# Optimization experiments

Measured on AMD Instinct MI355X. Metric: run time of the kernel, lower is better.

The kernel has to match this reference:

```python
import jax, jax.numpy as jnp
import numpy as np

S, B, E, H, NQ, V, T = 128, 128, 64, 8, 8, 30000, 12
N_RAND_OPS = 30


def _build_random_layer(n_wires, n_ops=N_RAND_OPS, seed=1234):
    # Deterministic stand-in for tq.RandomLayer(n_ops=30): random fixed-angle
    # rotations and CNOTs over the wires.
    rng = np.random.RandomState(seed)
    ops = []
    for _ in range(n_ops):
        kind = rng.randint(4)
        if kind == 3 and n_wires >= 2:
            c = int(rng.randint(n_wires))
            t = int(rng.randint(n_wires - 1))
            if t >= c:
                t += 1
            ops.append(('cnot', c, t, 0.0))
        else:
            g = ('rx', 'ry', 'rz')[kind % 3]
            ops.append((g, int(rng.randint(n_wires)), -1, float(rng.uniform(0.0, 2 * np.pi))))
    return ops

_RAND_OPS = _build_random_layer(H)


def _apply_rot(state, kind, theta, w):
    # state: (N, 2, 2, ..., 2); wire w lives on axis w+1. theta: scalar or (N,).
    th = jnp.asarray(theta, jnp.float32)
    if th.ndim == 1:
        th = th.reshape((-1,) + (1,) * (state.ndim - 2))
    th = th / 2
    a0 = jnp.take(state, 0, axis=w + 1)
    a1 = jnp.take(state, 1, axis=w + 1)
    c, s = jnp.cos(th), jnp.sin(th)
    if kind == 'rx':
        n0, n1 = c * a0 - 1j * s * a1, -1j * s * a0 + c * a1
    elif kind == 'ry':
        n0, n1 = c * a0 - s * a1, s * a0 + c * a1
    else:  # rz
        p = jnp.exp(-1j * th)
        n0, n1 = p * a0, jnp.conj(p) * a1
    return jnp.stack([n0, n1], axis=w + 1)


def _apply_cnot(state, c, t):
    s0 = jnp.take(state, 0, axis=c + 1)
    s1 = jnp.take(state, 1, axis=c + 1)
    t_ax = t + 1 if t < c else t  # target axis after removing control axis
    s1 = jnp.flip(s1, axis=t_ax)
    return jnp.stack([s0, s1], axis=c + 1)


def _measure_z(state):
    probs = jnp.real(state * jnp.conj(state))
    n = state.ndim - 1
    zs = []
    for w in range(n):
        d = jnp.take(probs, 0, axis=w + 1) - jnp.take(probs, 1, axis=w + 1)
        zs.append(d.sum(axis=tuple(range(1, d.ndim))))
    return jnp.stack(zs, axis=1)  # (N, n_wires)


def setup_inputs() -> dict:
    key = jax.random.key(0)
    ks = jax.random.split(key, 10)
    fan_lin = E + H
    return {
        'emb': jax.random.normal(ks[0], (V, E), jnp.float32),
        'Win': jax.random.normal(ks[1], (4, NQ, fan_lin), jnp.float32) / np.sqrt(fan_lin),
        'b_in': jax.random.normal(ks[2], (4, NQ), jnp.float32) * 0.1,
        'phi': jax.random.uniform(ks[3], (4, NQ), jnp.float32, 0.0, 2 * np.pi),
        'Wout': jax.random.normal(ks[4], (4, H, NQ), jnp.float32) / np.sqrt(NQ),
        'b_out': jax.random.normal(ks[5], (4, H), jnp.float32) * 0.1,
        'phiq': jax.random.uniform(ks[6], (H,), jnp.float32, 0.0, 2 * np.pi),
        'Whead': jax.random.normal(ks[7], (T, H), jnp.float32) / np.sqrt(H),
        'b_head': jax.random.normal(ks[8], (T,), jnp.float32) * 0.1,
        'sentence': jax.random.randint(ks[9], (S, B), 0, V, jnp.int64),
    }


def reference(emb, Win, b_in, phi, Wout, b_out, phiq, Whead, b_head, sentence):
    embeds = emb[sentence]  # (S, B, E)
    bsz = sentence.shape[1]
    h0 = jnp.zeros((bsz, H), emb.dtype)
    c0 = jnp.zeros_like(h0)

    def step(carry, x):
        hx, cx = carry
        comb = jnp.concatenate([x, hx], axis=1)  # (B, E+H)
        # QGate closed form: RX(z_i) encode + trainable RX(phi_i) + CNOT chain
        # gives <Z_k> = prod_{j<=k} cos(z_j + phi_j).
        z = jnp.einsum('bf,gqf->bgq', comb, Win) + b_in + phi  # (B,4,NQ)
        q = jnp.cumprod(jnp.cos(z), axis=-1)
        pre = jnp.einsum('bgq,ghq->bgh', q, Wout) + b_out      # (B,4,H)
        f = jax.nn.sigmoid(pre[:, 0])
        i = jax.nn.sigmoid(pre[:, 1])
        g = jnp.tanh(pre[:, 2])
        o = jax.nn.sigmoid(pre[:, 3])
        cx = f * cx + i * g
        hx = o * jnp.tanh(cx)
        return (hx, cx), hx

    _, outs = jax.lax.scan(step, (h0, c0), embeds)  # (S, B, H)
    flat = outs.transpose(1, 0, 2).reshape(-1, H)   # (B*S, H) batch-major (as in source)

    # QFC head: statevector simulation over H wires
    n = H
    N = flat.shape[0]
    state = jnp.zeros((N, 2 ** n), jnp.complex64).at[:, 0].set(1.0)
    state = state.reshape((N,) + (2,) * n)
    for w in range(n):
        state = _apply_rot(state, 'ry', flat[:, w], w)
    for name, a, b, ang in _RAND_OPS:
        if name == 'cnot':
            state = _apply_cnot(state, a, b)
        else:
            state = _apply_rot(state, name, ang, a)
    for w in range(n):
        state = _apply_rot(state, 'rx', phiq[w], w)
    zexp = _measure_z(state)                        # (B*S, H)
    logits = zexp @ Whead.T + b_head
    # faithful to source: view batch-major flat tensor as (seq, batch, T)
    logits = logits.reshape(S, B, T)
    return jax.nn.log_softmax(logits, axis=2)
```

## Files before the change

kernel.cpp:

```cpp
#include <hip/hip_runtime.h>
#include <math.h>
#include <stdint.h>

#define S_    128
#define B_    128
#define E_    64
#define H_    8
#define T_    12
#define FAN_  72
#define NOPS_ 30
#define MAXG_ 30
#define NROWS_ (S_ * B_)

constexpr double CT_PI = 3.14159265358979323846;

constexpr double ct_cos(double x) {
    double t = 1.0, s = 1.0, x2 = x * x;
    for (int k = 1; k <= 20; k++) { t *= -x2 / ((2.0*k - 1.0) * (2.0*k)); s += t; }
    return s;
}
constexpr double ct_sin(double x) {
    double t = x, s = x, x2 = x * x;
    for (int k = 1; k <= 20; k++) { t *= -x2 / ((2.0*k) * (2.0*k + 1.0)); s += t; }
    return s;
}

constexpr void ct_mmul(const double* A, const double* B, double* C) {
    for (int i = 0; i < 2; i++)
        for (int j = 0; j < 2; j++) {
            double rr = 0.0, ii = 0.0;
            for (int k = 0; k < 2; k++) {
                double ar = A[(i*2+k)*2], ai = A[(i*2+k)*2+1];
                double br = B[(k*2+j)*2], bi = B[(k*2+j)*2+1];
                rr += ar*br - ai*bi;
                ii += ar*bi + ai*br;
            }
            C[(i*2+j)*2] = rr; C[(i*2+j)*2+1] = ii;
        }
}

struct CTC {
    int n;
    int type[MAXG_];
    int w1[MAXG_];
    int w2[MAXG_];
    double U[MAXG_][8];
    double initM[8][8];
    double endM[8][8];
};

constexpr CTC build_ct() {
    uint32_t mt[624] = {};
    int idx = 624;
    {
        uint32_t s = 1234u;
        for (int i = 0; i < 624; i++) {
            mt[i] = s;
            s = 1812433253u * (s ^ (s >> 30)) + (uint32_t)i + 1u;
        }
    }
    auto nextf = [&]() -> uint32_t {
        if (idx >= 624) {
            for (int i = 0; i < 624; i++) {
                uint32_t y = (mt[i] & 0x80000000u) | (mt[(i+1)%624] & 0x7fffffffu);
                uint32_t v = mt[(i+397)%624] ^ (y >> 1);
                mt[i] = (y & 1u) ? (v ^ 0x9908b0dfu) : v;
            }
            idx = 0;
        }
        uint32_t y = mt[idx++];
        y ^= y >> 11;
        y ^= (y << 7)  & 0x9d2c5680u;
        y ^= (y << 15) & 0xefc60000u;
        y ^= y >> 18;
        return y;
    };
    auto randint = [&](uint32_t n) -> uint32_t {
        uint32_t rng = n - 1u, mask = rng;
        mask |= mask >> 1; mask |= mask >> 2; mask |= mask >> 4;
        mask |= mask >> 8; mask |= mask >> 16;
        uint32_t v = 0;
        do { v = nextf() & mask; } while (v > rng);
        return v;
    };
    auto uniform2pi = [&]() -> double {
        uint32_t a = nextf() >> 5;
        uint32_t b = nextf() >> 6;
        double d = ((double)a * 67108864.0 + (double)b) / 9007199254740992.0;
        return 2.0 * CT_PI * d;
    };

    int kindA[NOPS_] = {}, aA[NOPS_] = {}, bA[NOPS_] = {};
    double UA[NOPS_][8] = {};
    for (int i = 0; i < NOPS_; i++) {
        uint32_t kind = randint(4);
        if (kind == 3u) {
            int c = (int)randint(8);
            int t = (int)randint(7);
            if (t >= c) t += 1;
            kindA[i] = 1; aA[i] = c; bA[i] = t;
            UA[i][0] = 1.0; UA[i][6] = 1.0;
        } else {
            int g = (int)(kind % 3u);
            int w = (int)randint(8);
            double th = uniform2pi();
            double c = ct_cos(0.5 * th), s = ct_sin(0.5 * th);
            kindA[i] = 0; aA[i] = w; bA[i] = -1;
            if (g == 0)      { UA[i][0]=c;  UA[i][3]=-s; UA[i][5]=-s; UA[i][6]=c; }
            else if (g == 1) { UA[i][0]=c;  UA[i][2]=-s; UA[i][4]= s; UA[i][6]=c; }
            else             { UA[i][0]=c;  UA[i][1]=-s; UA[i][6]= c; UA[i][7]=s; }
        }
    }

    int ikind[MAXG_] = {}, ia[MAXG_] = {}, ib[MAXG_] = {};
    double iU[MAXG_][8] = {};
    int cnt = 0;
    double initM[8][8] = {}, endM[8][8] = {};
    for (int w = 0; w < 8; w++) { initM[w][0] = 1.0; initM[w][6] = 1.0;
                                  endM[w][0]  = 1.0; endM[w][6]  = 1.0; }

    for (int oi = 0; oi < NOPS_; oi++) {
        if (kindA[oi] == 0) {
            int w = aA[oi], k = cnt - 1;
            bool merged = false;
            while (k >= 0) {
                if (ikind[k] == 0) {
                    if (ia[k] == w) {
                        double tmp[8] = {};
                        ct_mmul(UA[oi], iU[k], tmp);
                        for (int j = 0; j < 8; j++) iU[k][j] = tmp[j];
                        merged = true; break;
                    }
                    k--;
                } else {
                    if (w == ia[k] || w == ib[k]) break;
                    k--;
                }
            }
            if (merged) continue;
            if (k < 0) {
                double tmp[8] = {};
                ct_mmul(UA[oi], initM[w], tmp);
                for (int j = 0; j < 8; j++) initM[w][j] = tmp[j];
                continue;
            }
            ikind[cnt] = 0; ia[cnt] = w; ib[cnt] = -1;
            for (int j = 0; j < 8; j++) iU[cnt][j] = UA[oi][j];
            cnt++;
        } else {
            int c = aA[oi], t2 = bA[oi], k = cnt - 1;
            bool cancelled = false;
            while (k >= 0) {
                if (ikind[k] == 0) {
                    int w = ia[k];
                    if (w == c || w == t2) break;
                    k--;
                } else {
                    int c2 = ia[k], tt = ib[k];
                    if (c2 == c && tt == t2) {
                        for (int m = k; m < cnt - 1; m++) {
                            ikind[m] = ikind[m+1]; ia[m] = ia[m+1]; ib[m] = ib[m+1];
                            for (int j = 0; j < 8; j++) iU[m][j] = iU[m+1][j];
                        }
                        cnt--; cancelled = true; break;
                    }
                    if (c2 != t2 && tt != c) k--;
                    else break;
                }
            }
            if (!cancelled) {
                ikind[cnt] = 1; ia[cnt] = c; ib[cnt] = t2;
                for (int j = 0; j < 8; j++) iU[cnt][j] = 0.0;
                iU[cnt][0] = 1.0; iU[cnt][6] = 1.0;
                cnt++;
            }
        }
    }
    bool blocked[8] = {};
    for (int k = cnt - 1; k >= 0; k--) {
        if (ikind[k] == 0) {
            int w = ia[k];
            if (!blocked[w]) {
                double tmp[8] = {};
                ct_mmul(endM[w], iU[k], tmp);
                for (int j = 0; j < 8; j++) endM[w][j] = tmp[j];
                for (int m = k; m < cnt - 1; m++) {
                    ikind[m] = ikind[m+1]; ia[m] = ia[m+1]; ib[m] = ib[m+1];
                    for (int j = 0; j < 8; j++) iU[m][j] = iU[m+1][j];
                }
                cnt--;
            }
        } else {
            blocked[ia[k]] = true; blocked[ib[k]] = true;
        }
    }

    CTC q = {};
    q.n = cnt;
    for (int i = 0; i < cnt; i++) {
        q.type[i] = ikind[i]; q.w1[i] = ia[i]; q.w2[i] = ib[i];
        for (int j = 0; j < 8; j++) q.U[i][j] = iU[i][j];
    }
    for (int w = 0; w < 8; w++)
        for (int j = 0; j < 8; j++) { q.initM[w][j] = initM[w][j]; q.endM[w][j] = endM[w][j]; }
    return q;
}

constexpr CTC CIRC = build_ct();

__device__ __forceinline__ float sigmoid_f(float x) { return 1.f / (1.f + __expf(-x)); }
__device__ __forceinline__ float tanh_f(float x) {
    float e = __expf(2.f * x);
    return 1.f - 2.f / (e + 1.f);
}

template<int CTRL>
__device__ __forceinline__ float dppf(float x) {
    union { float f; int i; } u, r;
    u.f = x;
    r.i = __builtin_amdgcn_update_dpp(0, u.i, CTRL, 0xF, 0xF, true);
    return r.f;
}

template<int M>
__device__ __forceinline__ float lane_xor(float x, int lane) {
    if constexpr (M == 1)  return dppf<0xB1>(x);
    else if constexpr (M == 2) return dppf<0x4E>(x);
    else if constexpr (M == 4) {
        float a = dppf<0x104>(x);
        float b = dppf<0x114>(x);
        return (lane & 4) ? b : a;
    }
    else if constexpr (M == 8) return dppf<0x128>(x);
    else return __shfl_xor(x, M, 64);
}

template<int W>
__device__ __forceinline__ float exch(float x, int lane) {
    if constexpr (W == 0) return __shfl_xor(x, 32, 64);
    else if constexpr (W == 1) return __shfl_xor(x, 16, 64);
    else if constexpr (W == 2) return lane_xor<8>(x, lane);
    else if constexpr (W == 3) return lane_xor<4>(x, lane);
    else if constexpr (W == 4) return lane_xor<2>(x, lane);
    else return lane_xor<1>(x, lane);
}

template<int W>
__device__ __forceinline__ int qbit_ct(int lane, int j) {
    if constexpr (W < 6) return (lane >> (5 - W)) & 1;
    else if constexpr (W == 6) return (j >> 1) & 1;
    else return j & 1;
}

__device__ __forceinline__ void pair_rt(float u0, float u1, float u2, float u3,
                                        float u4, float u5, float u6, float u7,
                                        float& a0r, float& a0i, float& a1r, float& a1i) {
    float n0r = u0*a0r - u1*a0i + u2*a1r - u3*a1i;
    float n0i = u0*a0i + u1*a0r + u2*a1i + u3*a1r;
    float n1r = u4*a0r - u5*a0i + u6*a1r - u7*a1i;
    float n1i = u4*a0i + u5*a0r + u6*a1i + u7*a1r;
    a0r = n0r; a0i = n0i; a1r = n1r; a1i = n1i;
}

template<int W>
__device__ __forceinline__ void gate_rt(float u0, float u1, float u2, float u3,
                                        float u4, float u5, float u6, float u7,
                                        int lane, float ar[4], float ai[4]) {
    if constexpr (W < 6) {
        const int b = (lane >> (5 - W)) & 1;
        const float dr  = b ? u6 : u0;
        const float di  = b ? u7 : u1;
        const float onr = b ? u4 : u2;
        const float oni = b ? u5 : u3;
        #pragma unroll
        for (int j = 0; j < 4; j++) {
            float br = exch<W>(ar[j], lane);
            float bi = exch<W>(ai[j], lane);
            float nr = dr * ar[j] - di * ai[j] + onr * br - oni * bi;
            float ni = dr * ai[j] + di * ar[j] + onr * bi + oni * br;
            ar[j] = nr; ai[j] = ni;
        }
    } else if constexpr (W == 6) {
        pair_rt(u0,u1,u2,u3,u4,u5,u6,u7, ar[0], ai[0], ar[2], ai[2]);
        pair_rt(u0,u1,u2,u3,u4,u5,u6,u7, ar[1], ai[1], ar[3], ai[3]);
    } else {
        pair_rt(u0,u1,u2,u3,u4,u5,u6,u7, ar[0], ai[0], ar[1], ai[1]);
        pair_rt(u0,u1,u2,u3,u4,u5,u6,u7, ar[2], ai[2], ar[3], ai[3]);
    }
}

template<int CW, int TW>
__device__ __forceinline__ void cnot_ct(int lane, float ar[4], float ai[4]) {
    if constexpr (TW < 6) {
        #pragma unroll
        for (int j = 0; j < 4; j++) {
            float br = exch<TW>(ar[j], lane);
            float bi = exch<TW>(ai[j], lane);
            int ctrl = qbit_ct<CW>(lane, j);
            ar[j] = ctrl ? br : ar[j];
            ai[j] = ctrl ? bi : ai[j];
        }
    } else if constexpr (TW == 6) {
        int cA = qbit_ct<CW>(lane, 0), cB = qbit_ct<CW>(lane, 1);
        float n0r = cA ? ar[2] : ar[0], n0i = cA ? ai[2] : ai[0];
        float n2r = cA ? ar[0] : ar[2], n2i = cA ? ai[0] : ai[2];
        float n1r = cB ? ar[3] : ar[1], n1i = cB ? ai[3] : ai[1];
        float n3r = cB ? ar[1] : ar[3], n3i = cB ? ai[1] : ai[3];
        ar[0]=n0r; ai[0]=n0i; ar[1]=n1r; ai[1]=n1i;
        ar[2]=n2r; ai[2]=n2i; ar[3]=n3r; ai[3]=n3i;
    } else {
        int cA = qbit_ct<CW>(lane, 0), cB = qbit_ct<CW>(lane, 2);
        float n0r = cA ? ar[1] : ar[0], n0i = cA ? ai[1] : ai[0];
        float n1r = cA ? ar[0] : ar[1], n1i = cA ? ai[0] : ai[1];
        float n2r = cB ? ar[3] : ar[2], n2i = cB ? ai[3] : ai[2];
        float n3r = cB ? ar[2] : ar[3], n3i = cB ? ai[2] : ai[3];
        ar[0]=n0r; ai[0]=n0i; ar[1]=n1r; ai[1]=n1i;
        ar[2]=n2r; ai[2]=n2i; ar[3]=n3r; ai[3]=n3i;
    }
}

template<int I>
__device__ __forceinline__ void gate_op(int lane, float ar[4], float ai[4]) {
    constexpr int w = CIRC.w1[I];
    constexpr float u0 = (float)CIRC.U[I][0], u1 = (float)CIRC.U[I][1];
    constexpr float u2 = (float)CIRC.U[I][2], u3 = (float)CIRC.U[I][3];
    constexpr float u4 = (float)CIRC.U[I][4], u5 = (float)CIRC.U[I][5];
    constexpr float u6 = (float)CIRC.U[I][6], u7 = (float)CIRC.U[I][7];
    gate_rt<w>(u0,u1,u2,u3,u4,u5,u6,u7, lane, ar, ai);
}

template<int I>
__device__ __forceinline__ void run_ops(int lane, float ar[4], float ai[4]) {
    if constexpr (I < CIRC.n) {
        if constexpr (CIRC.type[I] == 0) gate_op<I>(lane, ar, ai);
        else cnot_ct<CIRC.w1[I], CIRC.w2[I]>(lane, ar, ai);
        run_ops<I + 1>(lane, ar, ai);
    }
}

struct V2 { float r0, i0, r1, i1; };
template<int W>
__device__ __forceinline__ V2 init_wire(float th) {
    constexpr float m0 = (float)CIRC.initM[W][0], m1 = (float)CIRC.initM[W][1];
    constexpr float m2 = (float)CIRC.initM[W][2], m3 = (float)CIRC.initM[W][3];
    constexpr float m4 = (float)CIRC.initM[W][4], m5 = (float)CIRC.initM[W][5];
    constexpr float m6 = (float)CIRC.initM[W][6], m7 = (float)CIRC.initM[W][7];
    float c = __cosf(th), s = __sinf(th);
    V2 v;
    v.r0 = m0*c + m2*s; v.i0 = m1*c + m3*s;
    v.r1 = m4*c + m6*s; v.i1 = m5*c + m7*s;
    return v;
}

template<int W>
__device__ __forceinline__ void final_wire(float c, float s, int lane,
                                           float ar[4], float ai[4]) {
    constexpr float E0 = (float)CIRC.endM[W][0], E1 = (float)CIRC.endM[W][1];
    constexpr float E2 = (float)CIRC.endM[W][2], E3 = (float)CIRC.endM[W][3];
    constexpr float E4 = (float)CIRC.endM[W][4], E5 = (float)CIRC.endM[W][5];
    constexpr float E6 = (float)CIRC.endM[W][6], E7 = (float)CIRC.endM[W][7];
    float F0 =  c*E0 + s*E5;
    float F1 =  c*E1 - s*E4;
    float F2 =  c*E2 + s*E7;
    float F3 =  c*E3 - s*E6;
    float F4 =  s*E1 + c*E4;
    float F5 = -s*E0 + c*E5;
    float F6 =  s*E3 + c*E6;
    float F7 = -s*E2 + c*E7;
    gate_rt<W>(F0,F1,F2,F3,F4,F5,F6,F7, lane, ar, ai);
}

__device__ __forceinline__ void bcast8(float v, int lane, float h[8]) {
    float p  = lane_xor<1>(v, lane);
    float a0 = (lane & 1) ? p : v;
    float a1 = (lane & 1) ? v : p;
    float q0 = lane_xor<2>(a0, lane);
    float q1 = lane_xor<2>(a1, lane);
    float b0 = (lane & 2) ? q0 : a0;
    float b1 = (lane & 2) ? q1 : a1;
    float b2 = (lane & 2) ? a0 : q0;
    float b3 = (lane & 2) ? a1 : q1;
    float r0 = lane_xor<4>(b0, lane);
    float r1 = lane_xor<4>(b1, lane);
    float r2 = lane_xor<4>(b2, lane);
    float r3 = lane_xor<4>(b3, lane);
    h[0] = (lane & 4) ? r0 : b0;  h[1] = (lane & 4) ? r1 : b1;
    h[2] = (lane & 4) ? r2 : b2;  h[3] = (lane & 4) ? r3 : b3;
    h[4] = (lane & 4) ? b0 : r0;  h[5] = (lane & 4) ? b1 : r1;
    h[6] = (lane & 4) ? b2 : r2;  h[7] = (lane & 4) ? b3 : r3;
}

__device__ __forceinline__ void qfc_row(const float th[8],
    float cq[8], float sq[8], int lane,
    const float* __restrict__ Whead, const float* __restrict__ b_head,
    float* __restrict__ outrow)
{
    float ar[4], ai[4];
    {
        V2 v0 = init_wire<0>(th[0]);
        V2 v1 = init_wire<1>(th[1]);
        V2 v2 = init_wire<2>(th[2]);
        V2 v3 = init_wire<3>(th[3]);
        V2 v4 = init_wire<4>(th[4]);
        V2 v5 = init_wire<5>(th[5]);
        V2 v6 = init_wire<6>(th[6]);
        V2 v7 = init_wire<7>(th[7]);
        float Pr = 1.f, Pi = 0.f;
        {
            int bit = (lane >> 5) & 1;
            float er = bit ? v0.r1 : v0.r0, ei = bit ? v0.i1 : v0.i0;
            float nr = Pr*er - Pi*ei, ni = Pr*ei + Pi*er; Pr = nr; Pi = ni;
        }
        {
            int bit = (lane >> 4) & 1;
            float er = bit ? v1.r1 : v1.r0, ei = bit ? v1.i1 : v1.i0;
            float nr = Pr*er - Pi*ei, ni = Pr*ei + Pi*er; Pr = nr; Pi = ni;
        }
        {
            int bit = (lane >> 3) & 1;
            float er = bit ? v2.r1 : v2.r0, ei = bit ? v2.i1 : v2.i0;
            float nr = Pr*er - Pi*ei, ni = Pr*ei + Pi*er; Pr = nr; Pi = ni;
        }
        {
            int bit = (lane >> 2) & 1;
            float er = bit ? v3.r1 : v3.r0, ei = bit ? v3.i1 : v3.i0;
            float nr = Pr*er - Pi*ei, ni = Pr*ei + Pi*er; Pr = nr; Pi = ni;
        }
        {
            int bit = (lane >> 1) & 1;
            float er = bit ? v4.r1 : v4.r0, ei = bit ? v4.i1 : v4.i0;
            float nr = Pr*er - Pi*ei, ni = Pr*ei + Pi*er; Pr = nr; Pi = ni;
        }
        {
            int bit = lane & 1;
            float er = bit ? v5.r1 : v5.r0, ei = bit ? v5.i1 : v5.i0;
            float nr = Pr*er - Pi*ei, ni = Pr*ei + Pi*er; Pr = nr; Pi = ni;
        }
        float t0r = Pr*v6.r0 - Pi*v6.i0, t0i = Pr*v6.i0 + Pi*v6.r0;
        float t1r = Pr*v6.r1 - Pi*v6.i1, t1i = Pr*v6.i1 + Pi*v6.r1;
        ar[0] = t0r*v7.r0 - t0i*v7.i0;  ai[0] = t0r*v7.i0 + t0i*v7.r0;
        ar[1] = t0r*v7.r1 - t0i*v7.i1;  ai[1] = t0r*v7.i1 + t0i*v7.r1;
        ar[2] = t1r*v7.r0 - t1i*v7.i0;  ai[2] = t1r*v7.i0 + t1i*v7.r0;
        ar[3] = t1r*v7.r1 - t1i*v7.i1;  ai[3] = t1r*v7.i1 + t1i*v7.r1;
    }

    run_ops<0>(lane, ar, ai);

    final_wire<0>(cq[0], sq[0], lane, ar, ai);
    final_wire<1>(cq[1], sq[1], lane, ar, ai);
    final_wire<2>(cq[2], sq[2], lane, ar, ai);
    final_wire<3>(cq[3], sq[3], lane, ar, ai);
    final_wire<4>(cq[4], sq[4], lane, ar, ai);
    final_wire<5>(cq[5], sq[5], lane, ar, ai);
    final_wire<6>(cq[6], sq[6], lane, ar, ai);
    final_wire<7>(cq[7], sq[7], lane, ar, ai);

    float p0 = ar[0]*ar[0] + ai[0]*ai[0];
    float p1 = ar[1]*ar[1] + ai[1]*ai[1];
    float p2 = ar[2]*ar[2] + ai[2]*ai[2];
    float p3 = ar[3]*ar[3] + ai[3]*ai[3];
    float pt = p0 + p1 + p2 + p3;
    float a6 = p0 + p1 - p2 - p3;
    float a7 = p0 - p1 + p2 - p3;
    {
        float tv;
        tv = lane_xor<1>(pt, lane);  pt = (lane & 1)  ? (tv - pt) : (tv + pt);
        tv = lane_xor<2>(pt, lane);  pt = (lane & 2)  ? (tv - pt) : (tv + pt);
        tv = lane_xor<4>(pt, lane);  pt = (lane & 4)  ? (tv - pt) : (tv + pt);
        tv = lane_xor<8>(pt, lane);  pt = (lane & 8)  ? (tv - pt) : (tv + pt);
        tv = lane_xor<16>(pt, lane); pt = (lane & 16) ? (tv - pt) : (tv + pt);
        tv = lane_xor<32>(pt, lane); pt = (lane & 32) ? (tv - pt) : (tv + pt);
        a6 += lane_xor<1>(a6, lane);  a6 += lane_xor<2>(a6, lane);
        a6 += lane_xor<4>(a6, lane);  a6 += lane_xor<8>(a6, lane);
        a6 += lane_xor<16>(a6, lane); a6 += lane_xor<32>(a6, lane);
        a7 += lane_xor<1>(a7, lane);  a7 += lane_xor<2>(a7, lane);
        a7 += lane_xor<4>(a7, lane);  a7 += lane_xor<8>(a7, lane);
        a7 += lane_xor<16>(a7, lane); a7 += lane_xor<32>(a7, lane);
    }
    float zl[8];
    zl[0] = __shfl(pt, 32, 64);
    zl[1] = __shfl(pt, 16, 64);
    zl[2] = __shfl(pt, 8, 64);
    zl[3] = __shfl(pt, 4, 64);
    zl[4] = __shfl(pt, 2, 64);
    zl[5] = __shfl(pt, 1, 64);
    zl[6] = a6;
    zl[7] = a7;

    float logit = -1e30f;
    if (lane < T_) {
        logit = b_head[lane];
        #pragma unroll
        for (int w = 0; w < 8; w++)
            logit = fmaf(zl[w], Whead[lane * 8 + w], logit);
    }
    float mx = logit;
    mx = fmaxf(mx, lane_xor<1>(mx, lane));
    mx = fmaxf(mx, lane_xor<2>(mx, lane));
    mx = fmaxf(mx, lane_xor<4>(mx, lane));
    mx = fmaxf(mx, lane_xor<8>(mx, lane));
    float e = (lane < T_) ? __expf(logit - mx) : 0.f;
    float se = e;
    se += lane_xor<1>(se, lane);
    se += lane_xor<2>(se, lane);
    se += lane_xor<4>(se, lane);
    se += lane_xor<8>(se, lane);
    if (lane < T_)
        outrow[lane] = logit - mx - __logf(se);
}

__global__ __launch_bounds__(256) void k_lstm(
    const float* __restrict__ emb,
    const int* __restrict__ sentence,
    const float* __restrict__ Win,
    const float* __restrict__ b_in,
    const float* __restrict__ phi,
    const float* __restrict__ Wout,
    const float* __restrict__ b_out,
    float* __restrict__ angles)
{
    __shared__ float zxs[S_][32];

    const int t  = threadIdx.x;
    const int hw = t >> 5;
    const int l  = t & 31;
    const int b  = blockIdx.x;

    {
        const float4* w4 = (const float4*)(Win + l * FAN_);
        const float cb = b_in[l] + phi[l];

        #pragma unroll
        for (int kk = 0; kk < 4; kk++) {
            const int sb = hw * 16 + kk * 4;
            const float4* e4_0 = (const float4*)(emb + sentence[(sb + 0) * B_ + b] * E_);
            const float4* e4_1 = (const float4*)(emb + sentence[(sb + 1) * B_ + b] * E_);
            const float4* e4_2 = (const float4*)(emb + sentence[(sb + 2) * B_ + b] * E_);
            const float4* e4_3 = (const float4*)(emb + sentence[(sb + 3) * B_ + b] * E_);
            float a0 = cb, a1 = cb, a2 = cb, a3 = cb;
            #pragma unroll
            for (int f = 0; f < 16; f++) {
                float4 wv = w4[f];
                float4 x0 = e4_0[f];
                float4 x1 = e4_1[f];
                float4 x2 = e4_2[f];
                float4 x3 = e4_3[f];
                a0 = fmaf(x0.x, wv.x, a0); a0 = fmaf(x0.y, wv.y, a0);
                a0 = fmaf(x0.z, wv.z, a0); a0 = fmaf(x0.w, wv.w, a0);
                a1 = fmaf(x1.x, wv.x, a1); a1 = fmaf(x1.y, wv.y, a1);
                a1 = fmaf(x1.z, wv.z, a1); a1 = fmaf(x1.w, wv.w, a1);
                a2 = fmaf(x2.x, wv.x, a2); a2 = fmaf(x2.y, wv.y, a2);
                a2 = fmaf(x2.z, wv.z, a2); a2 = fmaf(x2.w, wv.w, a2);
                a3 = fmaf(x3.x, wv.x, a3); a3 = fmaf(x3.y, wv.y, a3);
                a3 = fmaf(x3.z, wv.z, a3); a3 = fmaf(x3.w, wv.w, a3);
            }
            zxs[sb + 0][l] = a0;
            zxs[sb + 1][l] = a1;
            zxs[sb + 2][l] = a2;
            zxs[sb + 3][l] = a3;
        }
    }
    __syncthreads();

    if (t < 32) {
        const int g = t >> 3;
        const int h = t & 7;
        const int q = t & 7;
        float wh[8], wo[8];
        #pragma unroll
        for (int k = 0; k < 8; k++) wh[k] = Win[t * FAN_ + 64 + k];
        #pragma unroll
        for (int k = 0; k < 8; k++) wo[k] = Wout[(g * 8 + h) * 8 + k];
        const float bo = b_out[g * 8 + h];

        float hxv[8];
        #pragma unroll
        for (int k = 0; k < 8; k++) hxv[k] = 0.f;
        float cx = 0.f;

        for (int s = 0; s < S_; s++) {
            float z = zxs[s][t];
            #pragma unroll
            for (int k = 0; k < 8; k++) z = fmaf(wh[k], hxv[k], z);

            float qc = __cosf(z);
            float u1 = dppf<0x111>(qc); qc = (q >= 1) ? qc * u1 : qc;
            float u2 = dppf<0x112>(qc); qc = (q >= 2) ? qc * u2 : qc;
            float u4 = dppf<0x114>(qc); qc = (q >= 4) ? qc * u4 : qc;

            float qch[8];
            bcast8(qc, t, qch);
            float pre = bo;
            #pragma unroll
            for (int qq = 0; qq < 8; qq++) pre = fmaf(wo[qq], qch[qq], pre);

            float e1 = lane_xor<8>(pre, t);
            float e2 = __shfl_xor(pre, 16, 64);
            float e3 = __shfl_xor(e1, 16, 64);
            float p0 = (g==0)?pre:(g==1)?e1:(g==2)?e2:e3;
            float p1 = (g==1)?pre:(g==0)?e1:(g==3)?e2:e3;
            float p2 = (g==2)?pre:(g==3)?e1:(g==0)?e2:e3;
            float p3 = (g==3)?pre:(g==2)?e1:(g==1)?e2:e3;

            float f_ = sigmoid_f(p0);
            float i_ = sigmoid_f(p1);
            float g_ = tanh_f(p2);
            float o_ = sigmoid_f(p3);
            cx = f_ * cx + i_ * g_;
            float hnew = o_ * tanh_f(cx);

            if (t < 8) angles[(b * S_ + s) * 8 + t] = hnew;
            bcast8(hnew, t, hxv);
        }
    }
}

__global__ __launch_bounds__(256) void k_qfc(
    const float* __restrict__ angles,
    const float* __restrict__ phiq,
    const float* __restrict__ Whead,
    const float* __restrict__ b_head,
    float* __restrict__ out)
{
    const int t      = threadIdx.x;
    const int lane   = t & 63;
    const int waveId = blockIdx.x * 4 + (t >> 6);

    float cq[8], sq[8];
    #pragma unroll
    for (int w = 0; w < 8; w++) {
        float ph = phiq[w] * 0.5f;
        cq[w] = __cosf(ph); sq[w] = __sinf(ph);
    }

    #pragma unroll
    for (int rr = 0; rr < 2; rr++) {
        const int row = waveId * 2 + rr;
        float th[8];
        #pragma unroll
        for (int w = 0; w < 8; w++) th[w] = angles[row * 8 + w] * 0.5f;
        qfc_row(th, cq, sq, lane, Whead, b_head, out + row * T_);
    }
}

__global__ __launch_bounds__(1024) void k_fused(
    const float* __restrict__ emb,
    const int* __restrict__ sentence,
    const float* __restrict__ Win,
    const float* __restrict__ b_in,
    const float* __restrict__ phi,
    const float* __restrict__ Wout,
    const float* __restrict__ b_out,
    const float* __restrict__ phiq,
    const float* __restrict__ Whead,
    const float* __restrict__ b_head,
    float* __restrict__ out)
{
    __shared__ float zxs[S_][32];
    __shared__ float sang[S_][8];

    const int t     = threadIdx.x;
    const int wave  = t >> 6;
    const int lane  = t & 63;
    const int half  = lane >> 5;
    const int l     = lane & 31;
    const int b     = blockIdx.x >> 1;
    const int half3 = blockIdx.x & 1;

    {
        const float4* w4 = (const float4*)(Win + l * FAN_);
        const float cb = b_in[l] + phi[l];
        const int s0 = wave * 8 + 0 + half;
        const int s1 = wave * 8 + 2 + half;
        const int s2 = wave * 8 + 4 + half;
        const int s3 = wave * 8 + 6 + half;
        const float4* e4_0 = (const float4*)(emb + sentence[s0 * B_ + b] * E_);
        const float4* e4_1 = (const float4*)(emb + sentence[s1 * B_ + b] * E_);
        const float4* e4_2 = (const float4*)(emb + sentence[s2 * B_ + b] * E_);
        const float4* e4_3 = (const float4*)(emb + sentence[s3 * B_ + b] * E_);
        float a0 = cb, a1 = cb, a2 = cb, a3 = cb;
        #pragma unroll
        for (int f = 0; f < 16; f++) {
            float4 wv = w4[f];
            float4 x0 = e4_0[f];
            float4 x1 = e4_1[f];
            float4 x2 = e4_2[f];
            float4 x3 = e4_3[f];
            a0 = fmaf(x0.x, wv.x, a0); a0 = fmaf(x0.y, wv.y, a0);
            a0 = fmaf(x0.z, wv.z, a0); a0 = fmaf(x0.w, wv.w, a0);
            a1 = fmaf(x1.x, wv.x, a1); a1 = fmaf(x1.y, wv.y, a1);
            a1 = fmaf(x1.z, wv.z, a1); a1 = fmaf(x1.w, wv.w, a1);
            a2 = fmaf(x2.x, wv.x, a2); a2 = fmaf(x2.y, wv.y, a2);
            a2 = fmaf(x2.z, wv.z, a2); a2 = fmaf(x2.w, wv.w, a2);
            a3 = fmaf(x3.x, wv.x, a3); a3 = fmaf(x3.y, wv.y, a3);
            a3 = fmaf(x3.z, wv.z, a3); a3 = fmaf(x3.w, wv.w, a3);
        }
        zxs[s0][l] = a0;
        zxs[s1][l] = a1;
        zxs[s2][l] = a2;
        zxs[s3][l] = a3;
    }
    __syncthreads();

    if (t < 32) {
        const int g = t >> 3;
        const int h = t & 7;
        const int q = t & 7;
        float wh[8], wo[8];
        #pragma unroll
        for (int k = 0; k < 8; k++) wh[k] = Win[t * FAN_ + 64 + k];
        #pragma unroll
        for (int k = 0; k < 8; k++) wo[k] = Wout[(g * 8 + h) * 8 + k];
        const float bo = b_out[g * 8 + h];

        float hxv[8];
        #pragma unroll
        for (int k = 0; k < 8; k++) hxv[k] = 0.f;
        float cx = 0.f;

        for (int s = 0; s < S_; s++) {
            float z = zxs[s][t];
            #pragma unroll
            for (int k = 0; k < 8; k++) z = fmaf(wh[k], hxv[k], z);

            float qc = __cosf(z);
            float u1 = dppf<0x111>(qc); qc = (q >= 1) ? qc * u1 : qc;
            float u2 = dppf<0x112>(qc); qc = (q >= 2) ? qc * u2 : qc;
            float u4 = dppf<0x114>(qc); qc = (q >= 4) ? qc * u4 : qc;

            float qch[8];
            bcast8(qc, t, qch);
            float pre = bo;
            #pragma unroll
            for (int qq = 0; qq < 8; qq++) pre = fmaf(wo[qq], qch[qq], pre);

            float e1 = lane_xor<8>(pre, t);
            float e2 = __shfl_xor(pre, 16, 64);
            float e3 = __shfl_xor(e1, 16, 64);
            float p0 = (g==0)?pre:(g==1)?e1:(g==2)?e2:e3;
            float p1 = (g==1)?pre:(g==0)?e1:(g==3)?e2:e3;
            float p2 = (g==2)?pre:(g==3)?e1:(g==0)?e2:e3;
            float p3 = (g==3)?pre:(g==2)?e1:(g==1)?e2:e3;

            float f_ = sigmoid_f(p0);
            float i_ = sigmoid_f(p1);
            float g_ = tanh_f(p2);
            float o_ = sigmoid_f(p3);
            cx = f_ * cx + i_ * g_;
            float hnew = o_ * tanh_f(cx);

            if (t < 8) sang[s][t] = hnew;
            bcast8(hnew, t, hxv);
        }
    }
    __syncthreads();

    float cq[8], sq[8];
    #pragma unroll
    for (int w = 0; w < 8; w++) {
        float ph = phiq[w] * 0.5f;
        cq[w] = __cosf(ph); sq[w] = __sinf(ph);
    }

    for (int r = 0; r < 4; r++) {
        const int s = half3 * 64 + wave * 4 + r;
        float th[8];
        #pragma unroll
        for (int w = 0; w < 8; w++) th[w] = sang[s][w] * 0.5f;
        qfc_row(th, cq, sq, lane, Whead, b_head, out + (b * S_ + s) * T_);
    }
}

extern "C" void kernel_launch(void* const* d_in, const int* in_sizes, int n_in,
                              void* d_out, int out_size, void* d_ws, size_t ws_size,
                              hipStream_t stream)
{
    (void)in_sizes; (void)n_in; (void)out_size;
    const float* emb    = (const float*)d_in[0];
    const float* Win    = (const float*)d_in[1];
    const float* b_in   = (const float*)d_in[2];
    const float* phi    = (const float*)d_in[3];
    const float* Wout   = (const float*)d_in[4];
    const float* b_out  = (const float*)d_in[5];
    const float* phiq   = (const float*)d_in[6];
    const float* Whead  = (const float*)d_in[7];
    const float* b_head = (const float*)d_in[8];
    const int* sentence = (const int*)d_in[9];
    float* out          = (float*)d_out;

    const size_t need = (size_t)NROWS_ * 8 * sizeof(float);
    if (ws_size >= need) {
        float* angles = (float*)d_ws;
        hipLaunchKernelGGL(k_lstm, dim3(B_), dim3(256), 0, stream,
                           emb, sentence, Win, b_in, phi, Wout, b_out, angles);
        hipLaunchKernelGGL(k_qfc, dim3(NROWS_ / 8), dim3(256), 0, stream,
                           angles, phiq, Whead, b_head, out);
    } else {
        hipLaunchKernelGGL(k_fused, dim3(2 * B_), dim3(1024), 0, stream,
                           emb, sentence, Win, b_in, phi, Wout, b_out,
                           phiq, Whead, b_head, out);
    }
}
```

Measured before the change: 191.2 us.

## Remap LSTM recurrence to 16 lanes with two gates per lane

The serial LSTM recurrence loop now runs on 16 lanes instead of 32. Each lane handles two gate rows, and the lane layout is interleaved so gate pairs can be exchanged with a single DPP swap instead of the multi-shuffle 4-way gather. The change also prefetches the next step's input projection from LDS and splits the dot-product FMA chains in two to shorten dependency latency. The goal is to cut cross-lane communication and latency on the sequential critical path, at the cost of doubling per-lane arithmetic and the broadcast work.

```diff
diff --git a/kernel.cpp b/kernel.cpp
--- a/kernel.cpp
+++ b/kernel.cpp
@@ -390,6 +390,26 @@
     h[6] = (lane & 4) ? b2 : r2;  h[7] = (lane & 4) ? b3 : r3;
 }
 
+__device__ __forceinline__ void bcast8_s2(float v, int lane, float h[8]) {
+    float p  = lane_xor<2>(v, lane);
+    float a0 = (lane & 2) ? p : v;
+    float a1 = (lane & 2) ? v : p;
+    float q0 = lane_xor<4>(a0, lane);
+    float q1 = lane_xor<4>(a1, lane);
+    float b0 = (lane & 4) ? q0 : a0;
+    float b1 = (lane & 4) ? q1 : a1;
+    float b2 = (lane & 4) ? a0 : q0;
+    float b3 = (lane & 4) ? a1 : q1;
+    float r0 = lane_xor<8>(b0, lane);
+    float r1 = lane_xor<8>(b1, lane);
+    float r2 = lane_xor<8>(b2, lane);
+    float r3 = lane_xor<8>(b3, lane);
+    h[0] = (lane & 8) ? r0 : b0;  h[1] = (lane & 8) ? r1 : b1;
+    h[2] = (lane & 8) ? r2 : b2;  h[3] = (lane & 8) ? r3 : b3;
+    h[4] = (lane & 8) ? b0 : r0;  h[5] = (lane & 8) ? b1 : r1;
+    h[6] = (lane & 8) ? b2 : r2;  h[7] = (lane & 8) ? b3 : r3;
+}
+
 __device__ __forceinline__ void qfc_row(const float th[8],
     float cq[8], float sq[8], int lane,
     const float* __restrict__ Whead, const float* __restrict__ b_head,
@@ -562,45 +582,79 @@
     }
     __syncthreads();
 
-    if (t < 32) {
-        const int g = t >> 3;
-        const int h = t & 7;
-        const int q = t & 7;
-        float wh[8], wo[8];
-        #pragma unroll
-        for (int k = 0; k < 8; k++) wh[k] = Win[t * FAN_ + 64 + k];
-        #pragma unroll
-        for (int k = 0; k < 8; k++) wo[k] = Wout[(g * 8 + h) * 8 + k];
-        const float bo = b_out[g * 8 + h];
+    if (t < 16) {
+        const int j = t & 1;
+        const int q = t >> 1;
+        const int rowA = j * 8 + q;
+        const int rowB = (j + 2) * 8 + q;
+
+        float whA[8], whB[8], woA[8], woB[8];
+        #pragma unroll
+        for (int k = 0; k < 8; k++) {
+            whA[k] = Win[rowA * FAN_ + 64 + k];
+            whB[k] = Win[rowB * FAN_ + 64 + k];
+            woA[k] = Wout[rowA * 8 + k];
+            woB[k] = Wout[rowB * 8 + k];
+        }
+        const float boA = b_out[rowA];
+        const float boB = b_out[rowB];
 
         float hxv[8];
         #pragma unroll
         for (int k = 0; k < 8; k++) hxv[k] = 0.f;
         float cx = 0.f;
 
+        float zAn = zxs[0][rowA];
+        float zBn = zxs[0][rowB];
+
         for (int s = 0; s < S_; s++) {
-            float z = zxs[s][t];
+            float zA = zAn, zB = zBn;
+            if (s + 1 < S_) {
+                zAn = zxs[s + 1][rowA];
+                zBn = zxs[s + 1][rowB];
+            }
+
+            float za0 = zA, za1 = 0.f, zb0 = zB, zb1 = 0.f;
             #pragma unroll
-            for (int k = 0; k < 8; k++) z = fmaf(wh[k], hxv[k], z);
-
-            float qc = __cosf(z);
-            float u1 = dppf<0x111>(qc); qc = (q >= 1) ? qc * u1 : qc;
-            float u2 = dppf<0x112>(qc); qc = (q >= 2) ? qc * u2 : qc;
-            float u4 = dppf<0x114>(qc); qc = (q >= 4) ? qc * u4 : qc;
-
-            float qch[8];
-            bcast8(qc, t, qch);
-            float pre = bo;
+            for (int k = 0; k < 4; k++) {
+                za0 = fmaf(whA[k], hxv[k], za0);
+                za1 = fmaf(whA[k + 4], hxv[k + 4], za1);
+                zb0 = fmaf(whB[k], hxv[k], zb0);
+                zb1 = fmaf(whB[k + 4], hxv[k + 4], zb1);
+            }
+            float qcA = __cosf(za0 + za1);
+            float qcB = __cosf(zb0 + zb1);
+
+            {
+                float uA = dppf<0x112>(qcA), uB = dppf<0x112>(qcB);
+                if (q >= 1) { qcA *= uA; qcB *= uB; }
+                uA = dppf<0x114>(qcA); uB = dppf<0x114>(qcB);
+                if (q >= 2) { qcA *= uA; qcB *= uB; }
+                uA = dppf<0x118>(qcA); uB = dppf<0x118>(qcB);
+                if (q >= 4) { qcA *= uA; qcB *= uB; }
+            }
+
+            float cA[8], cB[8];
+            bcast8_s2(qcA, t, cA);
+            bcast8_s2(qcB, t, cB);
+
+            float pa0 = boA, pa1 = 0.f, pb0 = boB, pb1 = 0.f;
             #pragma unroll
-            for (int qq = 0; qq < 8; qq++) pre = fmaf(wo[qq], qch[qq], pre);
-
-            float e1 = lane_xor<8>(pre, t);
-            float e2 = __shfl_xor(pre, 16, 64);
-            float e3 = __shfl_xor(e1, 16, 64);
-            float p0 = (g==0)?pre:(g==1)?e1:(g==2)?e2:e3;
-            float p1 = (g==1)?pre:(g==0)?e1:(g==3)?e2:e3;
-            float p2 = (g==2)?pre:(g==3)?e1:(g==0)?e2:e3;
-            float p3 = (g==3)?pre:(g==2)?e1:(g==1)?e2:e3;
+            for (int k = 0; k < 4; k++) {
+                pa0 = fmaf(woA[k], cA[k], pa0);
+                pa1 = fmaf(woA[k + 4], cA[k + 4], pa1);
+                pb0 = fmaf(woB[k], cB[k], pb0);
+                pb1 = fmaf(woB[k + 4], cB[k + 4], pb1);
+            }
+            float preA = pa0 + pa1;
+            float preB = pb0 + pb1;
+
+            float prA = dppf<0xB1>(preA);
+            float prB = dppf<0xB1>(preB);
+            float p0 = j ? prA  : preA;
+            float p1 = j ? preA : prA;
+            float p2 = j ? prB  : preB;
+            float p3 = j ? preB : prB;
 
             float f_ = sigmoid_f(p0);
             float i_ = sigmoid_f(p1);
@@ -609,8 +663,8 @@
             cx = f_ * cx + i_ * g_;
             float hnew = o_ * tanh_f(cx);
 
-            if (t < 8) angles[(b * S_ + s) * 8 + t] = hnew;
-            bcast8(hnew, t, hxv);
+            if (j == 0) angles[(b * S_ + s) * 8 + q] = hnew;
+            bcast8_s2(hnew, t, hxv);
         }
     }
 }
```

After: 197.5 us. 1.03x slower.
